# Performance work log

Hardware: AMD Instinct MI355X
Metric: run time of the kernel (lower is better)

## Reference

```python
import jax, jax.numpy as jnp
import numpy as np

B, H, W, C = 4, 64, 64, 1280
NH = 16          # num heads
HD = C // NH     # 80 features per head
WS = 14          # window size
REL = 2 * WS - 1 # 27 relative-position entries per axis
EPS = 1e-6


def setup_inputs() -> dict:
    key = jax.random.key(0)
    ks = jax.random.split(key, 16)
    s = 0.02
    return {
        "imagelike_bhwc": jax.random.normal(ks[0], (B, H, W, C), jnp.float32),
        "ln1_g": jnp.ones((C,), jnp.float32),
        "ln1_b": jnp.zeros((C,), jnp.float32),
        "qkv_w": jax.random.normal(ks[1], (C, 3 * C), jnp.float32) * s,
        "qkv_b": jnp.zeros((3 * C,), jnp.float32),
        "proj_w": jax.random.normal(ks[2], (C, C), jnp.float32) * s,
        "proj_b": jnp.zeros((C,), jnp.float32),
        "rel_pos_h": jax.random.normal(ks[3], (REL, HD), jnp.float32) * s,
        "rel_pos_w": jax.random.normal(ks[4], (REL, HD), jnp.float32) * s,
        "ln2_g": jnp.ones((C,), jnp.float32),
        "ln2_b": jnp.zeros((C,), jnp.float32),
        "mlp_w1": jax.random.normal(ks[5], (C, 4 * C), jnp.float32) * s,
        "mlp_b1": jnp.zeros((4 * C,), jnp.float32),
        "mlp_w2": jax.random.normal(ks[6], (4 * C, C), jnp.float32) * s,
        "mlp_b2": jnp.zeros((C,), jnp.float32),
    }


def _layernorm(t, g, b):
    mu = jnp.mean(t, axis=-1, keepdims=True)
    var = jnp.var(t, axis=-1, keepdims=True)
    return (t - mu) * jax.lax.rsqrt(var + EPS) * g + b


def reference(imagelike_bhwc, ln1_g, ln1_b, qkv_w, qkv_b, proj_w, proj_b,
              rel_pos_h, rel_pos_w, ln2_g, ln2_b, mlp_w1, mlp_b1, mlp_w2, mlp_b2):
    x = imagelike_bhwc
    b, h, w, c = x.shape
    hd = c // NH
    scale = hd ** -0.5
    # --- image -> windows (pad to multiple of WS) ---
    hp, wp = (-h) % WS, (-w) % WS
    xp = jnp.pad(x, ((0, 0), (0, hp), (0, wp), (0, 0)))
    Hp, Wp = h + hp, w + wp
    ny, nx = Hp // WS, Wp // WS
    win = xp.reshape(b, ny, WS, nx, WS, c).transpose(0, 1, 3, 2, 4, 5)
    win = win.reshape(b * ny * nx, WS, WS, c)      # (Bw, S, S, C)
    Bw, N = win.shape[0], WS * WS
    # --- pre-attention layernorm + qkv ---
    t = _layernorm(win, ln1_g, ln1_b)
    qkv = t.reshape(Bw, N, c) @ qkv_w + qkv_b      # (Bw, N, 3C)
    qkv = qkv.reshape(Bw, N, 3, NH, hd).transpose(2, 0, 3, 1, 4)  # (3,Bw,NH,N,hd)
    q, k, v = qkv[0], qkv[1], qkv[2]
    # --- scores + decomposed relative position bias ---
    attn = jnp.einsum('bhqd,bhkd->bhqk', q * scale, k)            # (Bw,NH,N,N)
    idx = jnp.arange(WS)[:, None] - jnp.arange(WS)[None, :] + (WS - 1)
    Rh = rel_pos_h[idx]                                           # (WS,WS,hd)
    Rw = rel_pos_w[idx]                                           # (WS,WS,hd)
    qr = q.reshape(Bw, NH, WS, WS, hd)
    bias_h = jnp.einsum('bnyxd,ykd->bnyxk', qr, Rh)               # (Bw,NH,WS,WS,WS)
    bias_w = jnp.einsum('bnyxd,xkd->bnyxk', qr, Rw)
    bias = (bias_h[..., :, None] + bias_w[..., None, :]).reshape(Bw, NH, N, N)
    attn = jax.nn.softmax(attn + bias, axis=-1)
    out = jnp.einsum('bhqk,bhkd->bhqd', attn, v)                  # (Bw,NH,N,hd)
    out = out.transpose(0, 2, 1, 3).reshape(Bw, WS, WS, c)
    out = out @ proj_w + proj_b
    attn_out = out + win                                          # residual 1
    # --- MLP ---
    t2 = _layernorm(attn_out, ln2_g, ln2_b)
    mlp = jax.nn.gelu(t2 @ mlp_w1 + mlp_b1, approximate=False) @ mlp_w2 + mlp_b2
    out = mlp + attn_out                                          # residual 2
    # --- windows -> image (remove padding) ---
    img = out.reshape(b, ny, nx, WS, WS, c).transpose(0, 1, 3, 2, 4, 5)
    img = img.reshape(b, Hp, Wp, c)
    return img[:, :h, :w, :]
```

## Files before the change

kernel.cpp:

```cpp
#include <hip/hip_runtime.h>

typedef __attribute__((ext_vector_type(8))) short short8;
typedef __attribute__((ext_vector_type(4))) float f32x4;

#define GLBP(p) ((const __attribute__((address_space(1))) void*)(p))
#define LDSP(p) ((__attribute__((address_space(3))) void*)(p))

__device__ __forceinline__ float bf2f(unsigned short u) {
  return __uint_as_float(((unsigned int)u) << 16);
}
__device__ __forceinline__ unsigned short f2bf(float f) {
  unsigned int u = __float_as_uint(f);
  u += 0x7fff + ((u >> 16) & 1);
  return (unsigned short)(u >> 16);
}

__device__ __forceinline__ void tok2pix(int gt, int& b, int& py, int& px) {
  int w = gt / 196, t = gt - w * 196;
  b = w / 25;
  int wr = w - b * 25;
  int wy = wr / 5, wx = wr - wy * 5;
  int ty = t / 14;
  py = wy * 14 + ty;
  px = wx * 14 + (t - ty * 14);
}

__global__ void k_transpose(const float* __restrict__ W, unsigned short* __restrict__ Wt,
                            int K, int N) {
  __shared__ float tile[32][33];
  int tx = threadIdx.x, ty = threadIdx.y;
  int n0 = blockIdx.x * 32, k0 = blockIdx.y * 32;
#pragma unroll
  for (int i = 0; i < 4; ++i)
    tile[ty + 8 * i][tx] = W[(size_t)(k0 + ty + 8 * i) * N + n0 + tx];
  __syncthreads();
#pragma unroll
  for (int i = 0; i < 4; ++i)
    Wt[(size_t)(n0 + ty + 8 * i) * K + k0 + tx] = f2bf(tile[tx][ty + 8 * i]);
}

__global__ __launch_bounds__(256) void k_ln1(const float* __restrict__ x,
                                             const float* __restrict__ g,
                                             const float* __restrict__ be,
                                             unsigned short* __restrict__ A1,
                                             int w0, int ctok) {
  int m = blockIdx.x * 4 + (threadIdx.x >> 6);
  int lane = threadIdx.x & 63;
  int b, py, px;
  tok2pix(w0 * 196 + m, b, py, px);
  bool valid = (m < ctok) && (py < 64) && (px < 64);
  const float* row = x + ((size_t)((b * 64 + py) * 64 + px)) * 1280;
  float v[20];
#pragma unroll
  for (int i = 0; i < 20; ++i) v[i] = valid ? row[lane + 64 * i] : 0.f;
  float s = 0.f, ss = 0.f;
#pragma unroll
  for (int i = 0; i < 20; ++i) { s += v[i]; ss += v[i] * v[i]; }
#pragma unroll
  for (int o = 32; o > 0; o >>= 1) { s += __shfl_down(s, o); ss += __shfl_down(ss, o); }
  s = __shfl(s, 0);
  ss = __shfl(ss, 0);
  float mu = s * (1.f / 1280.f);
  float var = ss * (1.f / 1280.f) - mu * mu;
  float rinv = rsqrtf(var + 1e-6f);
  unsigned short* o1 = A1 + (size_t)m * 1280;
#pragma unroll
  for (int i = 0; i < 20; ++i) {
    int c = lane + 64 * i;
    o1[c] = f2bf((v[i] - mu) * rinv * g[c] + be[c]);
  }
}

__global__ __launch_bounds__(256) void k_ln2(const unsigned short* __restrict__ AT,
                                             const float* __restrict__ g,
                                             const float* __restrict__ be,
                                             unsigned short* __restrict__ A2) {
  int m = blockIdx.x * 4 + (threadIdx.x >> 6);
  int lane = threadIdx.x & 63;
  const unsigned short* row = AT + (size_t)m * 1280;
  float v[20];
#pragma unroll
  for (int i = 0; i < 20; ++i) v[i] = bf2f(row[lane + 64 * i]);
  float s = 0.f, ss = 0.f;
#pragma unroll
  for (int i = 0; i < 20; ++i) { s += v[i]; ss += v[i] * v[i]; }
#pragma unroll
  for (int o = 32; o > 0; o >>= 1) { s += __shfl_down(s, o); ss += __shfl_down(ss, o); }
  s = __shfl(s, 0);
  ss = __shfl(ss, 0);
  float mu = s * (1.f / 1280.f);
  float var = ss * (1.f / 1280.f) - mu * mu;
  float rinv = rsqrtf(var + 1e-6f);
  unsigned short* o1 = A2 + (size_t)m * 1280;
#pragma unroll
  for (int i = 0; i < 20; ++i) {
    int c = lane + 64 * i;
    o1[c] = f2bf((v[i] - mu) * rinv * g[c] + be[c]);
  }
}

template <int EPI>
__device__ __forceinline__ void gemm_body(const unsigned short* __restrict__ A,
                                          const unsigned short* __restrict__ Bt,
                                          int K, int N, int gx,
                                          const float* __restrict__ bias,
                                          void* __restrict__ outp,
                                          const float* __restrict__ xres,
                                          const unsigned short* __restrict__ attnres,
                                          int w0, int ctok) {
  __shared__ __align__(16) char smem[73728];
  int tid = threadIdx.x;
  int w = tid >> 6, lane = tid & 63;
  int nwg = gridDim.x, bid = blockIdx.x;
  int q = nwg >> 3, r = nwg & 7;
  int xcd = bid & 7, loc = bid >> 3;
  int wg = (xcd < r ? xcd * (q + 1) : r * (q + 1) + (xcd - r) * q) + loc;
  int bx = wg % gx, by = wg / gx;
  int mBase = by * 256, nBase = bx * 128;
  int wr = w >> 2, wc = w & 3;
  int la = lane & 15, lg = lane >> 4;

  int srow = tid >> 2;
  int schunk = (tid & 3) ^ ((srow >> 1) & 3);
  const char* pa0 = (const char*)A + (size_t)(mBase + srow) * K * 2 + (schunk << 4);
  const char* pa1 = (const char*)A + (size_t)(mBase + 128 + srow) * K * 2 + (schunk << 4);
  const char* pb0 = (const char*)Bt + (size_t)(nBase + srow) * K * 2 + (schunk << 4);
  int ldst = tid * 16;

  auto STAGE = [&](int slot, size_t ko) {
    int b = slot * 24576;
    __builtin_amdgcn_global_load_lds(GLBP(pa0 + ko), LDSP(smem + b + ldst), 16, 0, 0);
    __builtin_amdgcn_global_load_lds(GLBP(pa1 + ko), LDSP(smem + b + 8192 + ldst), 16, 0, 0);
    __builtin_amdgcn_global_load_lds(GLBP(pb0 + ko), LDSP(smem + b + 16384 + ldst), 16, 0, 0);
  };

  int offA[8], offB[2];
#pragma unroll
  for (int m = 0; m < 8; ++m) {
    int rr = wr * 128 + m * 16 + la;
    offA[m] = rr * 64 + ((lg ^ ((rr >> 1) & 3)) << 4);
  }
#pragma unroll
  for (int n = 0; n < 2; ++n) {
    int rr = wc * 32 + n * 16 + la;
    offB[n] = 16384 + rr * 64 + ((lg ^ ((rr >> 1) & 3)) << 4);
  }

  const f32x4 z4 = {0.f, 0.f, 0.f, 0.f};
  f32x4 acc[8][2];
#pragma unroll
  for (int m = 0; m < 8; ++m)
#pragma unroll
    for (int n = 0; n < 2; ++n) acc[m][n] = z4;

  int NT = K >> 5;
  STAGE(0, 0);
  STAGE(1, 64);
  int rs = 0;
  for (int t = 0; t < NT; ++t) {
    if (t + 1 < NT)
      asm volatile("s_waitcnt vmcnt(3)" ::: "memory");
    else
      asm volatile("s_waitcnt vmcnt(0)" ::: "memory");
    __builtin_amdgcn_s_barrier();
    __builtin_amdgcn_sched_barrier(0);
    if (t + 2 < NT) {
      int ws = rs + 2;
      if (ws >= 3) ws -= 3;
      STAGE(ws, (size_t)(t + 2) * 64);
    }
    const char* buf = (const char*)smem + rs * 24576;
    short8 af[4], bfr[2];
#pragma unroll
    for (int n = 0; n < 2; ++n) bfr[n] = *(const short8*)(buf + offB[n]);
#pragma unroll
    for (int m = 0; m < 4; ++m) af[m] = *(const short8*)(buf + offA[m]);
    __builtin_amdgcn_s_setprio(1);
#pragma unroll
    for (int m = 0; m < 4; ++m)
#pragma unroll
      for (int n = 0; n < 2; ++n)
        acc[m][n] = __builtin_amdgcn_mfma_f32_16x16x32_bf16(af[m], bfr[n], acc[m][n], 0, 0, 0);
    __builtin_amdgcn_s_setprio(0);
    __builtin_amdgcn_sched_barrier(0);
#pragma unroll
    for (int m = 0; m < 4; ++m) af[m] = *(const short8*)(buf + offA[m + 4]);
    __builtin_amdgcn_s_setprio(1);
#pragma unroll
    for (int m = 0; m < 4; ++m)
#pragma unroll
      for (int n = 0; n < 2; ++n)
        acc[m + 4][n] = __builtin_amdgcn_mfma_f32_16x16x32_bf16(af[m], bfr[n], acc[m + 4][n], 0, 0, 0);
    __builtin_amdgcn_s_setprio(0);
    rs = (rs == 2) ? 0 : rs + 1;
  }

#pragma unroll
  for (int m = 0; m < 8; ++m) {
#pragma unroll
    for (int n = 0; n < 2; ++n) {
      int col = nBase + wc * 32 + n * 16 + la;
      float bcol = bias[col];
#pragma unroll
      for (int j = 0; j < 4; ++j) {
        int row = mBase + wr * 128 + m * 16 + lg * 4 + j;
        float v = acc[m][n][j] + bcol;
        if (EPI == 0) {
          if (row < ctok) {
            int wloc = row / 196, tt = row - wloc * 196;
            int which = col / 1280, cr = col - which * 1280;
            int nh = cr / 80, d = cr - nh * 80;
            ((unsigned short*)outp)[((((size_t)wloc * 16 + nh) * 3 + which) * 196 + tt) * 80 + d] =
                f2bf(v);
          }
        } else if (EPI == 2) {
          float gg = 0.5f * v * (1.f + erff(v * 0.70710678118654752f));
          ((unsigned short*)outp)[(size_t)row * N + col] = f2bf(gg);
        } else if (EPI == 1) {
          if (row < ctok) {
            int b, py, px;
            tok2pix(w0 * 196 + row, b, py, px);
            float wv = (py < 64 && px < 64)
                           ? xres[((size_t)((b * 64 + py) * 64 + px)) * 1280 + col]
                           : 0.f;
            ((unsigned short*)outp)[(size_t)row * 1280 + col] = f2bf(v + wv);
          }
        } else {
          if (row < ctok) {
            int b, py, px;
            tok2pix(w0 * 196 + row, b, py, px);
            if (py < 64 && px < 64)
              ((float*)outp)[((size_t)((b * 64 + py) * 64 + px)) * 1280 + col] =
                  v + bf2f(attnres[(size_t)row * 1280 + col]);
          }
        }
      }
    }
  }
}

__global__ __launch_bounds__(512, 4) void k_gqkv(const unsigned short* A, const unsigned short* Bt,
                                                 int K, int N, int gx, const float* bias, void* o,
                                                 const float* xr, const unsigned short* ar, int w0, int ct) {
  gemm_body<0>(A, Bt, K, N, gx, bias, o, xr, ar, w0, ct);
}
__global__ __launch_bounds__(512, 4) void k_gproj(const unsigned short* A, const unsigned short* Bt,
                                                  int K, int N, int gx, const float* bias, void* o,
                                                  const float* xr, const unsigned short* ar, int w0, int ct) {
  gemm_body<1>(A, Bt, K, N, gx, bias, o, xr, ar, w0, ct);
}
__global__ __launch_bounds__(512, 4) void k_gmlp1(const unsigned short* A, const unsigned short* Bt,
                                                  int K, int N, int gx, const float* bias, void* o,
                                                  const float* xr, const unsigned short* ar, int w0, int ct) {
  gemm_body<2>(A, Bt, K, N, gx, bias, o, xr, ar, w0, ct);
}
__global__ __launch_bounds__(512, 4) void k_gmlp2(const unsigned short* A, const unsigned short* Bt,
                                                  int K, int N, int gx, const float* bias, void* o,
                                                  const float* xr, const unsigned short* ar, int w0, int ct) {
  gemm_body<3>(A, Bt, K, N, gx, bias, o, xr, ar, w0, ct);
}

__global__ __launch_bounds__(512) void k_attn(const unsigned short* __restrict__ qkv,
                                              const float* __restrict__ rph,
                                              const float* __restrict__ rpw,
                                              unsigned short* __restrict__ AO, int cw) {
  int bid = blockIdx.x;
  int r = bid & 7, nh = (bid >> 3) & 15, a = bid >> 7;
  int w = 8 * a + r;
  if (w >= cw) return;

  __shared__ unsigned short Ks[208 * 104];
  __shared__ unsigned short Vt[80 * 248];
  __shared__ unsigned short Ps[8][16 * 248];
  __shared__ unsigned short Bls[196 * 28];
  int tid = threadIdx.x, wid = tid >> 6, lane = tid & 63;
  int la = lane & 15, lg = lane >> 4;
  const unsigned short* qb = qkv + ((size_t)(w * 16 + nh)) * 3 * 15680;
  const unsigned short* kb = qb + 15680;
  const unsigned short* vb = qb + 31360;
  const short8 z8 = {0, 0, 0, 0, 0, 0, 0, 0};

  for (int c = tid; c < 208 * 13; c += 512) {
    int t = c / 13, seg = c - t * 13;
    short8 kv = z8;
    if (t < 196 && seg < 10) kv = *(const short8*)(kb + (size_t)t * 80 + seg * 8);
    *(short8*)(Ks + t * 104 + seg * 8) = kv;
  }
  for (int c = tid; c < 196 * 10; c += 512) {
    int t = c / 10, d8 = (c - t * 10) * 8;
    short8 vv = *(const short8*)(vb + (size_t)t * 80 + d8);
#pragma unroll
    for (int e = 0; e < 8; ++e) Vt[(d8 + e) * 248 + t] = (unsigned short)vv[e];
  }
  for (int i = tid; i < 80 * 52; i += 512) Vt[(i / 52) * 248 + 196 + (i % 52)] = 0;
  for (int id = tid; id < 196 * 28; id += 512) {
    int t = id / 28, c = id - t * 28;
    int y = t / 14, xx = t - y * 14;
    const float* R = (c < 14) ? (rph + (size_t)(y - c + 13) * 80)
                              : (rpw + (size_t)(xx - (c - 14) + 13) * 80);
    const unsigned short* qq = qb + (size_t)t * 80;
    float acc = 0.f;
#pragma unroll
    for (int d8 = 0; d8 < 10; ++d8) {
      short8 qv = *(const short8*)(qq + d8 * 8);
      const float4* Rv = (const float4*)(R + d8 * 8);
      float4 ra = Rv[0], rb = Rv[1];
      acc += bf2f((unsigned short)qv[0]) * ra.x + bf2f((unsigned short)qv[1]) * ra.y +
             bf2f((unsigned short)qv[2]) * ra.z + bf2f((unsigned short)qv[3]) * ra.w +
             bf2f((unsigned short)qv[4]) * rb.x + bf2f((unsigned short)qv[5]) * rb.y +
             bf2f((unsigned short)qv[6]) * rb.z + bf2f((unsigned short)qv[7]) * rb.w;
    }
    Bls[id] = f2bf(acc);
  }
  __syncthreads();

  int kyv[13], kxv[13];
#pragma unroll
  for (int ci = 0; ci < 13; ++ci) {
    int key = ci * 16 + la;
    kyv[ci] = key / 14;
    kxv[ci] = key - kyv[ci] * 14;
  }

  const float scale = 0.111803398874989485f;
  const f32x4 z4 = {0.f, 0.f, 0.f, 0.f};
  unsigned short* P = Ps[wid];

  auto process = [&](int rb) {
    short8 qa[3];
#pragma unroll
    for (int kk = 0; kk < 3; ++kk) {
      int t = rb * 16 + la;
      int d = kk * 32 + lg * 8;
      qa[kk] = (t < 196 && d < 80) ? *(const short8*)(qb + (size_t)t * 80 + d) : z8;
    }
    f32x4 s[13];
#pragma unroll
    for (int i = 0; i < 13; ++i) s[i] = z4;
#pragma unroll
    for (int kk = 0; kk < 3; ++kk) {
#pragma unroll
      for (int ni = 0; ni < 13; ++ni) {
        short8 bb = *(const short8*)(Ks + (ni * 16 + la) * 104 + kk * 32 + lg * 8);
        s[ni] = __builtin_amdgcn_mfma_f32_16x16x32_bf16(qa[kk], bb, s[ni], 0, 0, 0);
      }
    }
#pragma unroll
    for (int j = 0; j < 4; ++j) {
      int rloc = lg * 4 + j;
      int t = rb * 16 + rloc;
      bool tval = t < 196;
      const unsigned short* Bp = Bls + (tval ? t : 0) * 28;
      float v[13];
      float mx = -3e30f;
#pragma unroll
      for (int ci = 0; ci < 13; ++ci) {
        int key = ci * 16 + la;
        float val = s[ci][j] * scale;
        if (key < 196 && tval) val += bf2f(Bp[kyv[ci]]) + bf2f(Bp[14 + kxv[ci]]);
        if (key >= 196) val = -3e30f;
        v[ci] = val;
        mx = fmaxf(mx, val);
      }
#pragma unroll
      for (int o = 1; o < 16; o <<= 1) mx = fmaxf(mx, __shfl_xor(mx, o));
      float sum = 0.f;
#pragma unroll
      for (int ci = 0; ci < 13; ++ci) {
        float e = __expf(v[ci] - mx);
        v[ci] = e;
        sum += e;
      }
#pragma unroll
      for (int o = 1; o < 16; o <<= 1) sum += __shfl_xor(sum, o);
      float inv = 1.f / sum;
#pragma unroll
      for (int ci = 0; ci < 13; ++ci) P[rloc * 248 + ci * 16 + la] = f2bf(v[ci] * inv);
      P[rloc * 248 + 208 + la] = 0;
    }
    f32x4 o5[5];
#pragma unroll
    for (int i = 0; i < 5; ++i) o5[i] = z4;
#pragma unroll
    for (int kc = 0; kc < 7; ++kc) {
      short8 aa = *(const short8*)(P + la * 248 + kc * 32 + lg * 8);
#pragma unroll
      for (int ni = 0; ni < 5; ++ni) {
        short8 bb = *(const short8*)(Vt + (ni * 16 + la) * 248 + kc * 32 + lg * 8);
        o5[ni] = __builtin_amdgcn_mfma_f32_16x16x32_bf16(aa, bb, o5[ni], 0, 0, 0);
      }
    }
#pragma unroll
    for (int ni = 0; ni < 5; ++ni)
#pragma unroll
      for (int j = 0; j < 4; ++j) {
        int t = rb * 16 + lg * 4 + j;
        if (t < 196)
          AO[((size_t)w * 196 + t) * 1280 + nh * 80 + ni * 16 + la] = f2bf(o5[ni][j]);
      }
  };

  process(wid);
  if (wid < 5) process(wid + 8);
}

extern "C" void kernel_launch(void* const* d_in, const int* in_sizes, int n_in,
                              void* d_out, int out_size, void* d_ws, size_t ws_size,
                              hipStream_t stream) {
  const float* x = (const float*)d_in[0];
  const float* ln1g = (const float*)d_in[1];
  const float* ln1b = (const float*)d_in[2];
  const float* qkvw = (const float*)d_in[3];
  const float* qkvb = (const float*)d_in[4];
  const float* projw = (const float*)d_in[5];
  const float* projb = (const float*)d_in[6];
  const float* rph = (const float*)d_in[7];
  const float* rpw = (const float*)d_in[8];
  const float* ln2g = (const float*)d_in[9];
  const float* ln2b = (const float*)d_in[10];
  const float* w1 = (const float*)d_in[11];
  const float* b1 = (const float*)d_in[12];
  const float* w2 = (const float*)d_in[13];
  const float* b2 = (const float*)d_in[14];
  float* out = (float*)d_out;

  const size_t woff = (3840ull * 1280 + 1280ull * 1280 + 5120ull * 1280 + 1280ull * 5120) * 2;
  const int NWopts[7] = {100, 50, 25, 10, 5, 2, 1};
  int NW = 0, Mb = 0;
  for (int i = 0; i < 7; ++i) {
    int nw = NWopts[i];
    int mb = ((nw * 196 + 255) / 256) * 256;
    size_t tot = woff + (size_t)mb * 2560  + (size_t)mb * 7680  +
                 (size_t)mb * 2560  + (size_t)mb * 2560 ;
    if (tot <= ws_size) { NW = nw; Mb = mb; break; }
  }
  if (!NW) return;

  char* p = (char*)d_ws;
  unsigned short* qkvwT = (unsigned short*)p; p += 3840ull * 1280 * 2;
  unsigned short* projwT = (unsigned short*)p; p += 1280ull * 1280 * 2;
  unsigned short* w1T = (unsigned short*)p; p += 5120ull * 1280 * 2;
  unsigned short* w2T = (unsigned short*)p; p += 1280ull * 5120 * 2;
  unsigned short* A1 = (unsigned short*)p; p += (size_t)Mb * 2560;
  unsigned short* QKV = (unsigned short*)p; p += (size_t)Mb * 7680;
  unsigned short* AO = (unsigned short*)p; p += (size_t)Mb * 2560;
  unsigned short* ATTN = (unsigned short*)p;
  unsigned short* Hb = QKV;
  unsigned short* A2 = A1;

  k_transpose<<<dim3(120, 40), dim3(32, 8), 0, stream>>>(qkvw, qkvwT, 1280, 3840);
  k_transpose<<<dim3(40, 40), dim3(32, 8), 0, stream>>>(projw, projwT, 1280, 1280);
  k_transpose<<<dim3(160, 40), dim3(32, 8), 0, stream>>>(w1, w1T, 1280, 5120);
  k_transpose<<<dim3(40, 160), dim3(32, 8), 0, stream>>>(w2, w2T, 5120, 1280);

  int gy = Mb / 256;
  int nchunks = (100 + NW - 1) / NW;
  for (int c = 0; c < nchunks; ++c) {
    int w0 = c * NW;
    int cw = (100 - w0 < NW) ? (100 - w0) : NW;
    int ctok = cw * 196;
    k_ln1<<<Mb / 4, 256, 0, stream>>>(x, ln1g, ln1b, A1, w0, ctok);
    k_gqkv<<<30 * gy, 512, 0, stream>>>(A1, qkvwT, 1280, 3840, 30, qkvb, (void*)QKV,
                                        nullptr, nullptr, 0, ctok);
    int ablk = ((cw + 7) / 8) * 128;
    k_attn<<<ablk, 512, 0, stream>>>(QKV, rph, rpw, AO, cw);
    k_gproj<<<10 * gy, 512, 0, stream>>>(AO, projwT, 1280, 1280, 10, projb, (void*)ATTN,
                                         x, nullptr, w0, ctok);
    k_ln2<<<Mb / 4, 256, 0, stream>>>(ATTN, ln2g, ln2b, A2);
    k_gmlp1<<<40 * gy, 512, 0, stream>>>(A2, w1T, 1280, 5120, 40, b1, (void*)Hb,
                                         nullptr, nullptr, 0, ctok);
    k_gmlp2<<<10 * gy, 512, 0, stream>>>(Hb, w2T, 5120, 1280, 10, b2, (void*)out,
                                         nullptr, ATTN, w0, ctok);
  }
}
```

Measured before the change: 1.603 ms.

## Split attention into rel-bias kernel and half-window blocks reading K from global

Moves the relative-position bias computation into its own kernel that writes the bias to a workspace buffer. The attention kernel now uses 256-thread blocks, each handling half of a window-head's query row-blocks, and reads K directly from global memory instead of staging it in LDS. This lowers LDS use so more blocks fit per CU. The chunking options are capped at 25 windows per chunk, which adds launches and a bias round-trip through memory in exchange.

```diff
diff --git a/kernel.cpp b/kernel.cpp
--- a/kernel.cpp
+++ b/kernel.cpp
@@ -260,40 +260,13 @@
   gemm_body<3>(A, Bt, K, N, gx, bias, o, xr, ar, w0, ct);
 }
 
-__global__ __launch_bounds__(512) void k_attn(const unsigned short* __restrict__ qkv,
-                                              const float* __restrict__ rph,
-                                              const float* __restrict__ rpw,
-                                              unsigned short* __restrict__ AO, int cw) {
-  int bid = blockIdx.x;
-  int r = bid & 7, nh = (bid >> 3) & 15, a = bid >> 7;
-  int w = 8 * a + r;
-  if (w >= cw) return;
-
-  __shared__ unsigned short Ks[208 * 104];
-  __shared__ unsigned short Vt[80 * 248];
-  __shared__ unsigned short Ps[8][16 * 248];
-  __shared__ unsigned short Bls[196 * 28];
-  int tid = threadIdx.x, wid = tid >> 6, lane = tid & 63;
-  int la = lane & 15, lg = lane >> 4;
-  const unsigned short* qb = qkv + ((size_t)(w * 16 + nh)) * 3 * 15680;
-  const unsigned short* kb = qb + 15680;
-  const unsigned short* vb = qb + 31360;
-  const short8 z8 = {0, 0, 0, 0, 0, 0, 0, 0};
-
-  for (int c = tid; c < 208 * 13; c += 512) {
-    int t = c / 13, seg = c - t * 13;
-    short8 kv = z8;
-    if (t < 196 && seg < 10) kv = *(const short8*)(kb + (size_t)t * 80 + seg * 8);
-    *(short8*)(Ks + t * 104 + seg * 8) = kv;
-  }
-  for (int c = tid; c < 196 * 10; c += 512) {
-    int t = c / 10, d8 = (c - t * 10) * 8;
-    short8 vv = *(const short8*)(vb + (size_t)t * 80 + d8);
-#pragma unroll
-    for (int e = 0; e < 8; ++e) Vt[(d8 + e) * 248 + t] = (unsigned short)vv[e];
-  }
-  for (int i = tid; i < 80 * 52; i += 512) Vt[(i / 52) * 248 + 196 + (i % 52)] = 0;
-  for (int id = tid; id < 196 * 28; id += 512) {
+__global__ __launch_bounds__(256) void k_relbias(const unsigned short* __restrict__ qkv,
+                                                 const float* __restrict__ rph,
+                                                 const float* __restrict__ rpw,
+                                                 unsigned short* __restrict__ B) {
+  int wh = blockIdx.x;
+  const unsigned short* qb = qkv + (size_t)wh * 47040;
+  for (int id = threadIdx.x; id < 196 * 28; id += 256) {
     int t = id / 28, c = id - t * 28;
     int y = t / 14, xx = t - y * 14;
     const float* R = (c < 14) ? (rph + (size_t)(y - c + 13) * 80)
@@ -310,8 +283,35 @@
              bf2f((unsigned short)qv[4]) * rb.x + bf2f((unsigned short)qv[5]) * rb.y +
              bf2f((unsigned short)qv[6]) * rb.z + bf2f((unsigned short)qv[7]) * rb.w;
     }
-    Bls[id] = f2bf(acc);
-  }
+    B[(size_t)wh * 5488 + id] = f2bf(acc);
+  }
+}
+
+__global__ __launch_bounds__(256, 2) void k_attn(const unsigned short* __restrict__ qkv,
+                                                 const unsigned short* __restrict__ Bias,
+                                                 unsigned short* __restrict__ AO) {
+  __shared__ unsigned short Vt[80 * 232];
+  __shared__ unsigned short Ps[4][16 * 232];
+  __shared__ unsigned short Bls[196 * 28];
+  int bid = blockIdx.x;
+  int half = bid & 1, wh = bid >> 1;
+  int w = wh >> 4, nh = wh & 15;
+  int tid = threadIdx.x, wid = tid >> 6, lane = tid & 63;
+  int la = lane & 15, lg = lane >> 4;
+  const unsigned short* qb = qkv + (size_t)wh * 47040;
+  const unsigned short* kb = qb + 15680;
+  const unsigned short* vb = qb + 31360;
+  const short8 z8 = {0, 0, 0, 0, 0, 0, 0, 0};
+
+  for (int c = tid; c < 1960; c += 256) {
+    int t = c / 10, d8 = (c - t * 10) * 8;
+    short8 vv = *(const short8*)(vb + (size_t)t * 80 + d8);
+#pragma unroll
+    for (int e = 0; e < 8; ++e) Vt[(d8 + e) * 232 + t] = (unsigned short)vv[e];
+  }
+  for (int i = tid; i < 80 * 36; i += 256) Vt[(i / 36) * 232 + 196 + (i % 36)] = 0;
+  for (int i = tid; i < 686; i += 256)
+    ((short8*)Bls)[i] = ((const short8*)(Bias + (size_t)wh * 5488))[i];
   __syncthreads();
 
   int kyv[13], kxv[13];
@@ -330,18 +330,18 @@
     short8 qa[3];
 #pragma unroll
     for (int kk = 0; kk < 3; ++kk) {
-      int t = rb * 16 + la;
       int d = kk * 32 + lg * 8;
-      qa[kk] = (t < 196 && d < 80) ? *(const short8*)(qb + (size_t)t * 80 + d) : z8;
+      qa[kk] = (kk < 2 || lg < 2) ? *(const short8*)(qb + (size_t)(rb * 16 + la) * 80 + d) : z8;
     }
     f32x4 s[13];
 #pragma unroll
     for (int i = 0; i < 13; ++i) s[i] = z4;
 #pragma unroll
     for (int kk = 0; kk < 3; ++kk) {
+      int d = kk * 32 + lg * 8;
 #pragma unroll
       for (int ni = 0; ni < 13; ++ni) {
-        short8 bb = *(const short8*)(Ks + (ni * 16 + la) * 104 + kk * 32 + lg * 8);
+        short8 bb = *(const short8*)(kb + (size_t)(ni * 16 + la) * 80 + d);
         s[ni] = __builtin_amdgcn_mfma_f32_16x16x32_bf16(qa[kk], bb, s[ni], 0, 0, 0);
       }
     }
@@ -358,7 +358,7 @@
         int key = ci * 16 + la;
         float val = s[ci][j] * scale;
         if (key < 196 && tval) val += bf2f(Bp[kyv[ci]]) + bf2f(Bp[14 + kxv[ci]]);
-        if (key >= 196) val = -3e30f;
+        if (key >= 196 || !tval) val = -3e30f;
         v[ci] = val;
         mx = fmaxf(mx, val);
       }
@@ -375,18 +375,18 @@
       for (int o = 1; o < 16; o <<= 1) sum += __shfl_xor(sum, o);
       float inv = 1.f / sum;
 #pragma unroll
-      for (int ci = 0; ci < 13; ++ci) P[rloc * 248 + ci * 16 + la] = f2bf(v[ci] * inv);
-      P[rloc * 248 + 208 + la] = 0;
+      for (int ci = 0; ci < 13; ++ci) P[rloc * 232 + ci * 16 + la] = f2bf(v[ci] * inv);
+      P[rloc * 232 + 208 + la] = 0;
     }
     f32x4 o5[5];
 #pragma unroll
     for (int i = 0; i < 5; ++i) o5[i] = z4;
 #pragma unroll
     for (int kc = 0; kc < 7; ++kc) {
-      short8 aa = *(const short8*)(P + la * 248 + kc * 32 + lg * 8);
+      short8 aa = *(const short8*)(P + la * 232 + kc * 32 + lg * 8);
 #pragma unroll
       for (int ni = 0; ni < 5; ++ni) {
-        short8 bb = *(const short8*)(Vt + (ni * 16 + la) * 248 + kc * 32 + lg * 8);
+        short8 bb = *(const short8*)(Vt + (ni * 16 + la) * 232 + kc * 32 + lg * 8);
         o5[ni] = __builtin_amdgcn_mfma_f32_16x16x32_bf16(aa, bb, o5[ni], 0, 0, 0);
       }
     }
@@ -400,8 +400,13 @@
       }
   };
 
-  process(wid);
-  if (wid < 5) process(wid + 8);
+  if (half == 0) {
+    process(wid);
+    if (wid < 3) process(wid + 4);
+  } else {
+    process(7 + wid);
+    if (wid < 2) process(11 + wid);
+  }
 }
 
 extern "C" void kernel_launch(void* const* d_in, const int* in_sizes, int n_in,
@@ -425,13 +430,12 @@
   float* out = (float*)d_out;
 
   const size_t woff = (3840ull * 1280 + 1280ull * 1280 + 5120ull * 1280 + 1280ull * 5120) * 2;
-  const int NWopts[7] = {100, 50, 25, 10, 5, 2, 1};
+  const int NWopts[10] = {25, 20, 16, 12, 10, 8, 5, 4, 2, 1};
   int NW = 0, Mb = 0;
-  for (int i = 0; i < 7; ++i) {
+  for (int i = 0; i < 10; ++i) {
     int nw = NWopts[i];
     int mb = ((nw * 196 + 255) / 256) * 256;
-    size_t tot = woff + (size_t)mb * 2560  + (size_t)mb * 7680  +
-                 (size_t)mb * 2560  + (size_t)mb * 2560 ;
+    size_t tot = woff + (size_t)mb * 15360 + (size_t)nw * 16 * 5488 * 2;
     if (tot <= ws_size) { NW = nw; Mb = mb; break; }
   }
   if (!NW) return;
@@ -444,7 +448,8 @@
   unsigned short* A1 = (unsigned short*)p; p += (size_t)Mb * 2560;
   unsigned short* QKV = (unsigned short*)p; p += (size_t)Mb * 7680;
   unsigned short* AO = (unsigned short*)p; p += (size_t)Mb * 2560;
-  unsigned short* ATTN = (unsigned short*)p;
+  unsigned short* ATTN = (unsigned short*)p; p += (size_t)Mb * 2560;
+  unsigned short* BIAS = (unsigned short*)p;
   unsigned short* Hb = QKV;
   unsigned short* A2 = A1;
 
@@ -462,8 +467,8 @@
     k_ln1<<<Mb / 4, 256, 0, stream>>>(x, ln1g, ln1b, A1, w0, ctok);
     k_gqkv<<<30 * gy, 512, 0, stream>>>(A1, qkvwT, 1280, 3840, 30, qkvb, (void*)QKV,
                                         nullptr, nullptr, 0, ctok);
-    int ablk = ((cw + 7) / 8) * 128;
-    k_attn<<<ablk, 512, 0, stream>>>(QKV, rph, rpw, AO, cw);
+    k_relbias<<<cw * 16, 256, 0, stream>>>(QKV, rph, rpw, BIAS);
+    k_attn<<<cw * 32, 256, 0, stream>>>(QKV, BIAS, AO);
     k_gproj<<<10 * gy, 512, 0, stream>>>(AO, projwT, 1280, 1280, 10, projb, (void*)ATTN,
                                          x, nullptr, w0, ctok);
     k_ln2<<<Mb / 4, 256, 0, stream>>>(ATTN, ln2g, ln2b, A2);
```

Measured after the change: 1.899 ms. 18.5% more time.

## Use 128x128 GEMM tiles for proj/MLP2, keep residual in fp32 output, smaller chunks

Applied to the files above, without the earlier changes.

The proj and MLP2 GEMMs move to a new 128x128-tile, 256-thread kernel with a 3-stage LDS pipeline, which gives more workgroups for these N=1280 GEMMs. The attention residual is now written straight into the fp32 output image and read back by LN2 and MLP2, which drops the bf16 ATTN buffer and one rounding step. Attention launches one block per window-head, with smaller LDS padding and masked invalid query rows. Chunk sizes now top out at 25 windows, presumably to keep intermediates cache-resident, at the cost of more kernel launches.

```diff
diff --git a/kernel.cpp b/kernel.cpp
--- a/kernel.cpp
+++ b/kernel.cpp
@@ -71,16 +71,20 @@
   }
 }
 
-__global__ __launch_bounds__(256) void k_ln2(const unsigned short* __restrict__ AT,
+__global__ __launch_bounds__(256) void k_ln2(const float* __restrict__ AT,
                                              const float* __restrict__ g,
                                              const float* __restrict__ be,
-                                             unsigned short* __restrict__ A2) {
+                                             unsigned short* __restrict__ A2,
+                                             int w0, int ctok) {
   int m = blockIdx.x * 4 + (threadIdx.x >> 6);
   int lane = threadIdx.x & 63;
-  const unsigned short* row = AT + (size_t)m * 1280;
+  int b, py, px;
+  tok2pix(w0 * 196 + m, b, py, px);
+  bool valid = (m < ctok) && (py < 64) && (px < 64);
+  const float* row = AT + ((size_t)((b * 64 + py) * 64 + px)) * 1280;
   float v[20];
 #pragma unroll
-  for (int i = 0; i < 20; ++i) v[i] = bf2f(row[lane + 64 * i]);
+  for (int i = 0; i < 20; ++i) v[i] = valid ? row[lane + 64 * i] : 0.f;
   float s = 0.f, ss = 0.f;
 #pragma unroll
   for (int i = 0; i < 20; ++i) { s += v[i]; ss += v[i] * v[i]; }
@@ -104,10 +108,7 @@
                                           const unsigned short* __restrict__ Bt,
                                           int K, int N, int gx,
                                           const float* __restrict__ bias,
-                                          void* __restrict__ outp,
-                                          const float* __restrict__ xres,
-                                          const unsigned short* __restrict__ attnres,
-                                          int w0, int ctok) {
+                                          void* __restrict__ outp, int ctok) {
   __shared__ __align__(16) char smem[73728];
   int tid = threadIdx.x;
   int w = tid >> 6, lane = tid & 63;
@@ -213,25 +214,126 @@
             ((unsigned short*)outp)[((((size_t)wloc * 16 + nh) * 3 + which) * 196 + tt) * 80 + d] =
                 f2bf(v);
           }
-        } else if (EPI == 2) {
+        } else {
           float gg = 0.5f * v * (1.f + erff(v * 0.70710678118654752f));
           ((unsigned short*)outp)[(size_t)row * N + col] = f2bf(gg);
-        } else if (EPI == 1) {
-          if (row < ctok) {
-            int b, py, px;
-            tok2pix(w0 * 196 + row, b, py, px);
-            float wv = (py < 64 && px < 64)
-                           ? xres[((size_t)((b * 64 + py) * 64 + px)) * 1280 + col]
-                           : 0.f;
-            ((unsigned short*)outp)[(size_t)row * 1280 + col] = f2bf(v + wv);
-          }
-        } else {
-          if (row < ctok) {
-            int b, py, px;
-            tok2pix(w0 * 196 + row, b, py, px);
-            if (py < 64 && px < 64)
-              ((float*)outp)[((size_t)((b * 64 + py) * 64 + px)) * 1280 + col] =
-                  v + bf2f(attnres[(size_t)row * 1280 + col]);
+        }
+      }
+    }
+  }
+}
+
+template <int EPI>
+__device__ __forceinline__ void gemm128_body(const unsigned short* __restrict__ A,
+                                             const unsigned short* __restrict__ Bt,
+                                             int K, int N, int gx,
+                                             const float* __restrict__ bias,
+                                             float* __restrict__ outp,
+                                             const float* __restrict__ xres,
+                                             int w0, int ctok) {
+  __shared__ __align__(16) char smem[49152];
+  int tid = threadIdx.x;
+  int w = tid >> 6, lane = tid & 63;
+  int nwg = gridDim.x, bid = blockIdx.x;
+  int q = nwg >> 3, r = nwg & 7;
+  int xcd = bid & 7, loc = bid >> 3;
+  int wg = (xcd < r ? xcd * (q + 1) : r * (q + 1) + (xcd - r) * q) + loc;
+  int bx = wg % gx, by = wg / gx;
+  int mBase = by * 128, nBase = bx * 128;
+  int wr = w >> 1, wc = w & 1;
+  int la = lane & 15, lg = lane >> 4;
+
+  int srow = tid >> 2;
+  int schunk = (tid & 3) ^ ((srow >> 1) & 3);
+  const char* pa[2];
+  const char* pb[2];
+#pragma unroll
+  for (int i = 0; i < 2; ++i) {
+    pa[i] = (const char*)A + (size_t)(mBase + srow + i * 64) * K * 2 + (schunk << 4);
+    pb[i] = (const char*)Bt + (size_t)(nBase + srow + i * 64) * K * 2 + (schunk << 4);
+  }
+  int ldst = tid * 16;
+
+  auto STAGE = [&](int slot, size_t ko) {
+    int b = slot * 16384;
+#pragma unroll
+    for (int i = 0; i < 2; ++i)
+      __builtin_amdgcn_global_load_lds(GLBP(pa[i] + ko), LDSP(smem + b + i * 4096 + ldst), 16, 0, 0);
+#pragma unroll
+    for (int i = 0; i < 2; ++i)
+      __builtin_amdgcn_global_load_lds(GLBP(pb[i] + ko), LDSP(smem + b + 8192 + i * 4096 + ldst), 16, 0, 0);
+  };
+
+  int offA[4], offB[4];
+#pragma unroll
+  for (int m = 0; m < 4; ++m) {
+    int rr = wr * 64 + m * 16 + la;
+    offA[m] = rr * 64 + ((lg ^ ((rr >> 1) & 3)) << 4);
+  }
+#pragma unroll
+  for (int n = 0; n < 4; ++n) {
+    int rr = wc * 64 + n * 16 + la;
+    offB[n] = 8192 + rr * 64 + ((lg ^ ((rr >> 1) & 3)) << 4);
+  }
+
+  const f32x4 z4 = {0.f, 0.f, 0.f, 0.f};
+  f32x4 acc[4][4];
+#pragma unroll
+  for (int m = 0; m < 4; ++m)
+#pragma unroll
+    for (int n = 0; n < 4; ++n) acc[m][n] = z4;
+
+  int NT = K >> 5;
+  STAGE(0, 0);
+  STAGE(1, 64);
+  int rs = 0;
+  for (int t = 0; t < NT; ++t) {
+    if (t + 1 < NT)
+      asm volatile("s_waitcnt vmcnt(4)" ::: "memory");
+    else
+      asm volatile("s_waitcnt vmcnt(0)" ::: "memory");
+    __builtin_amdgcn_s_barrier();
+    __builtin_amdgcn_sched_barrier(0);
+    if (t + 2 < NT) {
+      int ws = rs + 2;
+      if (ws >= 3) ws -= 3;
+      STAGE(ws, (size_t)(t + 2) * 64);
+    }
+    const char* buf = (const char*)smem + rs * 16384;
+    short8 af[4], bfr[4];
+#pragma unroll
+    for (int n = 0; n < 4; ++n) bfr[n] = *(const short8*)(buf + offB[n]);
+#pragma unroll
+    for (int m = 0; m < 4; ++m) af[m] = *(const short8*)(buf + offA[m]);
+    __builtin_amdgcn_s_setprio(1);
+#pragma unroll
+    for (int m = 0; m < 4; ++m)
+#pragma unroll
+      for (int n = 0; n < 4; ++n)
+        acc[m][n] = __builtin_amdgcn_mfma_f32_16x16x32_bf16(af[m], bfr[n], acc[m][n], 0, 0, 0);
+    __builtin_amdgcn_s_setprio(0);
+    rs = (rs == 2) ? 0 : rs + 1;
+  }
+
+#pragma unroll
+  for (int m = 0; m < 4; ++m) {
+#pragma unroll
+    for (int n = 0; n < 4; ++n) {
+      int col = nBase + wc * 64 + n * 16 + la;
+      float bcol = bias[col];
+#pragma unroll
+      for (int j = 0; j < 4; ++j) {
+        int row = mBase + wr * 64 + m * 16 + lg * 4 + j;
+        if (row < ctok) {
+          int b, py, px;
+          tok2pix(w0 * 196 + row, b, py, px);
+          if (py < 64 && px < 64) {
+            size_t pix = ((size_t)((b * 64 + py) * 64 + px)) * 1280 + col;
+            float v = acc[m][n][j] + bcol;
+            if (EPI == 1)
+              outp[pix] = v + xres[pix];
+            else
+              outp[pix] = v + outp[pix];
           }
         }
       }
@@ -241,41 +343,38 @@
 
 __global__ __launch_bounds__(512, 4) void k_gqkv(const unsigned short* A, const unsigned short* Bt,
                                                  int K, int N, int gx, const float* bias, void* o,
-                                                 const float* xr, const unsigned short* ar, int w0, int ct) {
-  gemm_body<0>(A, Bt, K, N, gx, bias, o, xr, ar, w0, ct);
-}
-__global__ __launch_bounds__(512, 4) void k_gproj(const unsigned short* A, const unsigned short* Bt,
-                                                  int K, int N, int gx, const float* bias, void* o,
-                                                  const float* xr, const unsigned short* ar, int w0, int ct) {
-  gemm_body<1>(A, Bt, K, N, gx, bias, o, xr, ar, w0, ct);
+                                                 int ct) {
+  gemm_body<0>(A, Bt, K, N, gx, bias, o, ct);
 }
 __global__ __launch_bounds__(512, 4) void k_gmlp1(const unsigned short* A, const unsigned short* Bt,
                                                   int K, int N, int gx, const float* bias, void* o,
-                                                  const float* xr, const unsigned short* ar, int w0, int ct) {
-  gemm_body<2>(A, Bt, K, N, gx, bias, o, xr, ar, w0, ct);
-}
-__global__ __launch_bounds__(512, 4) void k_gmlp2(const unsigned short* A, const unsigned short* Bt,
-                                                  int K, int N, int gx, const float* bias, void* o,
-                                                  const float* xr, const unsigned short* ar, int w0, int ct) {
-  gemm_body<3>(A, Bt, K, N, gx, bias, o, xr, ar, w0, ct);
-}
-
-__global__ __launch_bounds__(512) void k_attn(const unsigned short* __restrict__ qkv,
-                                              const float* __restrict__ rph,
-                                              const float* __restrict__ rpw,
-                                              unsigned short* __restrict__ AO, int cw) {
-  int bid = blockIdx.x;
-  int r = bid & 7, nh = (bid >> 3) & 15, a = bid >> 7;
-  int w = 8 * a + r;
-  if (w >= cw) return;
-
+                                                  int ct) {
+  gemm_body<2>(A, Bt, K, N, gx, bias, o, ct);
+}
+__global__ __launch_bounds__(256, 3) void k_gproj(const unsigned short* A, const unsigned short* Bt,
+                                                  int K, int N, int gx, const float* bias, float* o,
+                                                  const float* xr, int w0, int ct) {
+  gemm128_body<1>(A, Bt, K, N, gx, bias, o, xr, w0, ct);
+}
+__global__ __launch_bounds__(256, 3) void k_gmlp2(const unsigned short* A, const unsigned short* Bt,
+                                                  int K, int N, int gx, const float* bias, float* o,
+                                                  const float* xr, int w0, int ct) {
+  gemm128_body<3>(A, Bt, K, N, gx, bias, o, xr, w0, ct);
+}
+
+__global__ __launch_bounds__(512, 1) void k_attn(const unsigned short* __restrict__ qkv,
+                                                 const float* __restrict__ rph,
+                                                 const float* __restrict__ rpw,
+                                                 unsigned short* __restrict__ AO) {
   __shared__ unsigned short Ks[208 * 104];
-  __shared__ unsigned short Vt[80 * 248];
-  __shared__ unsigned short Ps[8][16 * 248];
+  __shared__ unsigned short Vt[80 * 232];
+  __shared__ unsigned short Ps[8][16 * 232];
   __shared__ unsigned short Bls[196 * 28];
+  int wh = blockIdx.x;
+  int w = wh >> 4, nh = wh & 15;
   int tid = threadIdx.x, wid = tid >> 6, lane = tid & 63;
   int la = lane & 15, lg = lane >> 4;
-  const unsigned short* qb = qkv + ((size_t)(w * 16 + nh)) * 3 * 15680;
+  const unsigned short* qb = qkv + (size_t)wh * 47040;
   const unsigned short* kb = qb + 15680;
   const unsigned short* vb = qb + 31360;
   const short8 z8 = {0, 0, 0, 0, 0, 0, 0, 0};
@@ -286,13 +385,13 @@
     if (t < 196 && seg < 10) kv = *(const short8*)(kb + (size_t)t * 80 + seg * 8);
     *(short8*)(Ks + t * 104 + seg * 8) = kv;
   }
-  for (int c = tid; c < 196 * 10; c += 512) {
+  for (int c = tid; c < 1960; c += 512) {
     int t = c / 10, d8 = (c - t * 10) * 8;
     short8 vv = *(const short8*)(vb + (size_t)t * 80 + d8);
 #pragma unroll
-    for (int e = 0; e < 8; ++e) Vt[(d8 + e) * 248 + t] = (unsigned short)vv[e];
-  }
-  for (int i = tid; i < 80 * 52; i += 512) Vt[(i / 52) * 248 + 196 + (i % 52)] = 0;
+    for (int e = 0; e < 8; ++e) Vt[(d8 + e) * 232 + t] = (unsigned short)vv[e];
+  }
+  for (int i = tid; i < 80 * 36; i += 512) Vt[(i / 36) * 232 + 196 + (i % 36)] = 0;
   for (int id = tid; id < 196 * 28; id += 512) {
     int t = id / 28, c = id - t * 28;
     int y = t / 14, xx = t - y * 14;
@@ -328,11 +427,12 @@
 
   auto process = [&](int rb) {
     short8 qa[3];
+    int tq = rb * 16 + la;
+    if (tq >= 196) tq = 0;
 #pragma unroll
     for (int kk = 0; kk < 3; ++kk) {
-      int t = rb * 16 + la;
       int d = kk * 32 + lg * 8;
-      qa[kk] = (t < 196 && d < 80) ? *(const short8*)(qb + (size_t)t * 80 + d) : z8;
+      qa[kk] = (kk < 2 || lg < 2) ? *(const short8*)(qb + (size_t)tq * 80 + d) : z8;
     }
     f32x4 s[13];
 #pragma unroll
@@ -358,7 +458,7 @@
         int key = ci * 16 + la;
         float val = s[ci][j] * scale;
         if (key < 196 && tval) val += bf2f(Bp[kyv[ci]]) + bf2f(Bp[14 + kxv[ci]]);
-        if (key >= 196) val = -3e30f;
+        if (key >= 196 || !tval) val = -3e30f;
         v[ci] = val;
         mx = fmaxf(mx, val);
       }
@@ -375,18 +475,18 @@
       for (int o = 1; o < 16; o <<= 1) sum += __shfl_xor(sum, o);
       float inv = 1.f / sum;
 #pragma unroll
-      for (int ci = 0; ci < 13; ++ci) P[rloc * 248 + ci * 16 + la] = f2bf(v[ci] * inv);
-      P[rloc * 248 + 208 + la] = 0;
+      for (int ci = 0; ci < 13; ++ci) P[rloc * 232 + ci * 16 + la] = f2bf(v[ci] * inv);
+      P[rloc * 232 + 208 + la] = 0;
     }
     f32x4 o5[5];
 #pragma unroll
     for (int i = 0; i < 5; ++i) o5[i] = z4;
 #pragma unroll
     for (int kc = 0; kc < 7; ++kc) {
-      short8 aa = *(const short8*)(P + la * 248 + kc * 32 + lg * 8);
+      short8 aa = *(const short8*)(P + la * 232 + kc * 32 + lg * 8);
 #pragma unroll
       for (int ni = 0; ni < 5; ++ni) {
-        short8 bb = *(const short8*)(Vt + (ni * 16 + la) * 248 + kc * 32 + lg * 8);
+        short8 bb = *(const short8*)(Vt + (ni * 16 + la) * 232 + kc * 32 + lg * 8);
         o5[ni] = __builtin_amdgcn_mfma_f32_16x16x32_bf16(aa, bb, o5[ni], 0, 0, 0);
       }
     }
@@ -425,13 +525,12 @@
   float* out = (float*)d_out;
 
   const size_t woff = (3840ull * 1280 + 1280ull * 1280 + 5120ull * 1280 + 1280ull * 5120) * 2;
-  const int NWopts[7] = {100, 50, 25, 10, 5, 2, 1};
+  const int NWopts[12] = {25, 20, 18, 16, 14, 12, 10, 8, 5, 4, 2, 1};
   int NW = 0, Mb = 0;
-  for (int i = 0; i < 7; ++i) {
+  for (int i = 0; i < 12; ++i) {
     int nw = NWopts[i];
     int mb = ((nw * 196 + 255) / 256) * 256;
-    size_t tot = woff + (size_t)mb * 2560  + (size_t)mb * 7680  +
-                 (size_t)mb * 2560  + (size_t)mb * 2560 ;
+    size_t tot = woff + (size_t)mb * 12800;
     if (tot <= ws_size) { NW = nw; Mb = mb; break; }
   }
   if (!NW) return;
@@ -443,8 +542,7 @@
   unsigned short* w2T = (unsigned short*)p; p += 1280ull * 5120 * 2;
   unsigned short* A1 = (unsigned short*)p; p += (size_t)Mb * 2560;
   unsigned short* QKV = (unsigned short*)p; p += (size_t)Mb * 7680;
-  unsigned short* AO = (unsigned short*)p; p += (size_t)Mb * 2560;
-  unsigned short* ATTN = (unsigned short*)p;
+  unsigned short* AO = (unsigned short*)p;
   unsigned short* Hb = QKV;
   unsigned short* A2 = A1;
 
@@ -453,23 +551,18 @@
   k_transpose<<<dim3(160, 40), dim3(32, 8), 0, stream>>>(w1, w1T, 1280, 5120);
   k_transpose<<<dim3(40, 160), dim3(32, 8), 0, stream>>>(w2, w2T, 5120, 1280);
 
-  int gy = Mb / 256;
+  int gy256 = Mb / 256, gy128 = Mb / 128;
   int nchunks = (100 + NW - 1) / NW;
   for (int c = 0; c < nchunks; ++c) {
     int w0 = c * NW;
     int cw = (100 - w0 < NW) ? (100 - w0) : NW;
     int ctok = cw * 196;
     k_ln1<<<Mb / 4, 256, 0, stream>>>(x, ln1g, ln1b, A1, w0, ctok);
-    k_gqkv<<<30 * gy, 512, 0, stream>>>(A1, qkvwT, 1280, 3840, 30, qkvb, (void*)QKV,
-                                        nullptr, nullptr, 0, ctok);
-    int ablk = ((cw + 7) / 8) * 128;
-    k_attn<<<ablk, 512, 0, stream>>>(QKV, rph, rpw, AO, cw);
-    k_gproj<<<10 * gy, 512, 0, stream>>>(AO, projwT, 1280, 1280, 10, projb, (void*)ATTN,
-                                         x, nullptr, w0, ctok);
-    k_ln2<<<Mb / 4, 256, 0, stream>>>(ATTN, ln2g, ln2b, A2);
-    k_gmlp1<<<40 * gy, 512, 0, stream>>>(A2, w1T, 1280, 5120, 40, b1, (void*)Hb,
-                                         nullptr, nullptr, 0, ctok);
-    k_gmlp2<<<10 * gy, 512, 0, stream>>>(Hb, w2T, 5120, 1280, 10, b2, (void*)out,
-                                         nullptr, ATTN, w0, ctok);
-  }
-}
+    k_gqkv<<<30 * gy256, 512, 0, stream>>>(A1, qkvwT, 1280, 3840, 30, qkvb, (void*)QKV, ctok);
+    k_attn<<<cw * 16, 512, 0, stream>>>(QKV, rph, rpw, AO);
+    k_gproj<<<10 * gy128, 256, 0, stream>>>(AO, projwT, 1280, 1280, 10, projb, out, x, w0, ctok);
+    k_ln2<<<Mb / 4, 256, 0, stream>>>(out, ln2g, ln2b, A2, w0, ctok);
+    k_gmlp1<<<40 * gy256, 512, 0, stream>>>(A2, w1T, 1280, 5120, 40, b1, (void*)Hb, ctok);
+    k_gmlp2<<<10 * gy128, 256, 0, stream>>>(Hb, w2T, 5120, 1280, 10, b2, out, nullptr, w0, ctok);
+  }
+}
```

Result: slower. 1.873 ms (+16.8%).
